# Kernel optimization log

Hardware: AMD Instinct MI355X
Metric: run time of the kernel (lower is better)

The kernel has to match this reference:

```python
import jax, jax.numpy as jnp
import numpy as np

D_MODEL = 512; N_HEADS = 8; HEAD = D_MODEL // N_HEADS; D_FF = 2048
N_LAYERS = 4; VOCAB = 32000; B = 2; S = 1024; T = 1024


def _posenc(seq_len, d_model):
    pos = np.arange(seq_len)[:, None].astype(np.float32)
    div = np.exp(np.arange(0, d_model, 2).astype(np.float32) * (-np.log(10000.0) / d_model))
    pe = np.zeros((seq_len, d_model), dtype=np.float32)
    pe[:, 0::2] = np.sin(pos * div)
    pe[:, 1::2] = np.cos(pos * div)
    return jnp.asarray(pe)


def _layernorm(x, g, b, eps=1e-6):
    mean = x.mean(-1, keepdims=True)
    xc = x - mean
    # torch .var() is unbiased (ddof=1) -- replicate exactly
    var = (xc * xc).sum(-1, keepdims=True) / (x.shape[-1] - 1)
    return g * (xc * (var + eps) ** -0.5) + b


def _mha(q, k, v, w, mask):
    # w: [4, D, D] stacked (W_q, W_k, W_v, W_o), applied as x @ W
    def heads(x, wi):
        return (x @ wi).reshape(x.shape[0], x.shape[1], N_HEADS, HEAD).transpose(0, 2, 1, 3)
    Q, K, V = heads(q, w[0]), heads(k, w[1]), heads(v, w[2])  # [B,H,S,hd]
    att = jnp.einsum('bhqd,bhkd->bhqk', Q, K) * HEAD ** (-0.5)
    att = jnp.where(mask == 0, -jnp.inf, att)
    att = jax.nn.softmax(att, axis=-1)
    y = jnp.einsum('bhqk,bhkd->bhqd', att, V)
    y = y.transpose(0, 2, 1, 3).reshape(q.shape[0], q.shape[1], D_MODEL)
    return y @ w[3]


def _ff(x, w1, b1, w2, b2):
    return jax.nn.relu(x @ w1 + b1) @ w2 + b2


def setup_inputs() -> dict:
    key = jax.random.key(0)
    ks = iter(jax.random.split(key, 32))
    std = 0.02
    inp = {}
    inp['src'] = jax.random.randint(next(ks), (B, S), 0, VOCAB)
    inp['tgt'] = jax.random.randint(next(ks), (B, T), 0, VOCAB)
    inp['src_mask'] = jnp.ones((B, 1, 1, S), dtype=jnp.int32)
    inp['tgt_mask'] = jnp.tril(jnp.ones((T, T), dtype=jnp.int32))[None, None].repeat(B, axis=0)
    inp['src_emb'] = jax.random.normal(next(ks), (VOCAB, D_MODEL)) * std
    inp['tgt_emb'] = jax.random.normal(next(ks), (VOCAB, D_MODEL)) * std
    inp['enc_att_w'] = jax.random.normal(next(ks), (N_LAYERS, 4, D_MODEL, D_MODEL)) * std
    inp['enc_ff_w1'] = jax.random.normal(next(ks), (N_LAYERS, D_MODEL, D_FF)) * std
    inp['enc_ff_b1'] = jnp.zeros((N_LAYERS, D_FF))
    inp['enc_ff_w2'] = jax.random.normal(next(ks), (N_LAYERS, D_FF, D_MODEL)) * std
    inp['enc_ff_b2'] = jnp.zeros((N_LAYERS, D_MODEL))
    inp['enc_norm_g'] = jnp.ones((N_LAYERS, 2, D_MODEL))
    inp['enc_norm_b'] = jnp.zeros((N_LAYERS, 2, D_MODEL))
    inp['enc_final_g'] = jnp.ones((D_MODEL,))
    inp['enc_final_b'] = jnp.zeros((D_MODEL,))
    inp['dec_att_w'] = jax.random.normal(next(ks), (N_LAYERS, 2, 4, D_MODEL, D_MODEL)) * std
    inp['dec_ff_w1'] = jax.random.normal(next(ks), (N_LAYERS, D_MODEL, D_FF)) * std
    inp['dec_ff_b1'] = jnp.zeros((N_LAYERS, D_FF))
    inp['dec_ff_w2'] = jax.random.normal(next(ks), (N_LAYERS, D_FF, D_MODEL)) * std
    inp['dec_ff_b2'] = jnp.zeros((N_LAYERS, D_MODEL))
    inp['dec_norm_g'] = jnp.ones((N_LAYERS, 3, D_MODEL))
    inp['dec_norm_b'] = jnp.zeros((N_LAYERS, 3, D_MODEL))
    inp['dec_final_g'] = jnp.ones((D_MODEL,))
    inp['dec_final_b'] = jnp.zeros((D_MODEL,))
    inp['proj_w'] = jax.random.normal(next(ks), (D_MODEL, VOCAB)) * std
    inp['proj_b'] = jnp.zeros((VOCAB,))
    return inp


def reference(src, tgt, src_mask, tgt_mask, src_emb, tgt_emb,
              enc_att_w, enc_ff_w1, enc_ff_b1, enc_ff_w2, enc_ff_b2,
              enc_norm_g, enc_norm_b, enc_final_g, enc_final_b,
              dec_att_w, dec_ff_w1, dec_ff_b1, dec_ff_w2, dec_ff_b2,
              dec_norm_g, dec_norm_b, dec_final_g, dec_final_b,
              proj_w, proj_b):
    scale = jnp.float32(np.sqrt(D_MODEL))
    # Encoder (pre-norm residuals: x = x + layer(norm(x)); dropout=0)
    x = src_emb[src] * scale + _posenc(S, D_MODEL)[None]
    for i in range(N_LAYERS):
        z = _layernorm(x, enc_norm_g[i, 0], enc_norm_b[i, 0])
        x = x + _mha(z, z, z, enc_att_w[i], src_mask)
        z = _layernorm(x, enc_norm_g[i, 1], enc_norm_b[i, 1])
        x = x + _ff(z, enc_ff_w1[i], enc_ff_b1[i], enc_ff_w2[i], enc_ff_b2[i])
    enc = _layernorm(x, enc_final_g, enc_final_b)
    # Decoder
    y = tgt_emb[tgt] * scale + _posenc(T, D_MODEL)[None]
    for i in range(N_LAYERS):
        z = _layernorm(y, dec_norm_g[i, 0], dec_norm_b[i, 0])
        y = y + _mha(z, z, z, dec_att_w[i, 0], tgt_mask)
        z = _layernorm(y, dec_norm_g[i, 1], dec_norm_b[i, 1])
        y = y + _mha(z, enc, enc, dec_att_w[i, 1], src_mask)
        z = _layernorm(y, dec_norm_g[i, 2], dec_norm_b[i, 2])
        y = y + _ff(z, dec_ff_w1[i], dec_ff_b1[i], dec_ff_w2[i], dec_ff_b2[i])
    dec = _layernorm(y, dec_final_g, dec_final_b)
    return dec @ proj_w + proj_b  # [B, T, VOCAB] logits
```

## Files before the change

### kernel.cpp

```cpp
#include <hip/hip_runtime.h>
#include <hip/hip_bf16.h>
#include <math.h>

#define D_MODEL 512
#define N_HEADS 8
#define HEAD 64
#define D_FF   2048
#define N_LAYERS 4
#define VOCAB  32000
#define BATCH  2
#define SEQ    1024

typedef __attribute__((ext_vector_type(8))) short bf16x8;
typedef __attribute__((ext_vector_type(4))) float f32x4;

__device__ __forceinline__ float b2f(short s) {
    unsigned int u = ((unsigned int)(unsigned short)s) << 16;
    float f; __builtin_memcpy(&f, &u, 4);
    return f;
}
__device__ __forceinline__ short f2b(float f) {
    __hip_bfloat16 h = __float2bfloat16(f);
    unsigned short u; __builtin_memcpy(&u, &h, 2);
    return (short)u;
}
__device__ __forceinline__ void storev(float* p, float v) { *p = v; }
__device__ __forceinline__ void storev(short* p, float v) { *p = f2b(v); }

__device__ __forceinline__ void transT_tile(const float* __restrict__ s,
                                            short* __restrict__ d,
                                            int K, int N, int tx, int ty, int tid) {
    __shared__ float t[64][65];
    int r = tid >> 2, c4 = (tid & 3) * 4;
#pragma unroll
    for (int jj = 0; jj < 4; ++jj) {
        int col = c4 + jj * 16;
        *(float4*)&t[r][col] = *(const float4*)(s + (size_t)(ty * 64 + r) * N + tx * 64 + col);
    }
    __syncthreads();
#pragma unroll
    for (int jj = 0; jj < 4; ++jj) {
        int kc = c4 + jj * 16;
        short4 o = make_short4(f2b(t[kc][r]), f2b(t[kc + 1][r]),
                               f2b(t[kc + 2][r]), f2b(t[kc + 3][r]));
        *(short4*)(d + (size_t)(tx * 64 + r) * K + ty * 64 + kc) = o;
    }
}

__global__ __launch_bounds__(256) void transT_kernel(const float* __restrict__ src,
                                                     short* __restrict__ dst,
                                                     int K, int N) {
    const float* s = src + (size_t)blockIdx.z * K * N;
    short* d = dst + (size_t)blockIdx.z * K * N;
    transT_tile(s, d, K, N, blockIdx.x, blockIdx.y, threadIdx.x);
}

__global__ __launch_bounds__(256) void repack_attT_kernel(const float* __restrict__ encw,
                                                          const float* __restrict__ decw,
                                                          short* __restrict__ w_enc_qkv,
                                                          short* __restrict__ w_dec_qkv,
                                                          short* __restrict__ w_dec_kv,
                                                          short* __restrict__ w_o) {
    int z = blockIdx.y;
    const float* s; short* d;
    if (z < 12)      { int i = z / 3, j = z % 3;
                       s = encw + (size_t)(i * 4 + j) * 262144;
                       d = w_enc_qkv + (size_t)i * 786432 + j * 262144; }
    else if (z < 24) { int u = z - 12, i = u / 3, j = u % 3;
                       s = decw + (size_t)(i * 8 + j) * 262144;
                       d = w_dec_qkv + (size_t)i * 786432 + j * 262144; }
    else if (z < 32) { int u = z - 24, i = u / 2, j = u % 2;
                       s = decw + (size_t)(i * 8 + 5 + j) * 262144;
                       d = w_dec_kv + (size_t)i * 524288 + j * 262144; }
    else             { int u = z - 32; const float* b; int mi;
                       if (u < 4)       { b = encw; mi = u * 4 + 3; }
                       else if (u < 8)  { b = decw; mi = (u - 4) * 8 + 3; }
                       else if (u < 12) { b = decw; mi = (u - 8) * 8 + 4; }
                       else             { b = decw; mi = (u - 12) * 8 + 7; }
                       s = b + (size_t)mi * 262144; d = w_o + (size_t)u * 262144; }
    int bx = blockIdx.x;
    transT_tile(s, d, 512, 512, bx & 7, bx >> 3, threadIdx.x);
}

__global__ void embed_kernel(const int* __restrict__ tokA, const int* __restrict__ tokB,
                             const float* __restrict__ embA, const float* __restrict__ embB,
                             float* __restrict__ outA, float* __restrict__ outB) {
    int row = blockIdx.x;
    const int* tok = blockIdx.y ? tokB : tokA;
    const float* emb = blockIdx.y ? embB : embA;
    float* out = blockIdx.y ? outB : outA;
    int s = row % SEQ;
    int token = tok[row];
    const float scale = 22.627416997969522f;
    const float c = -1.7988945941359737e-2f;
    for (int d = threadIdx.x; d < D_MODEL; d += blockDim.x) {
        int i2 = (d >> 1) * 2;
        float div = expf((float)i2 * c);
        float ang = (float)s * div;
        float pe = (d & 1) ? cosf(ang) : sinf(ang);
        out[(size_t)row * D_MODEL + d] = emb[(size_t)token * D_MODEL + d] * scale + pe;
    }
}

__global__ __launch_bounds__(256) void ln_kernel(const float* __restrict__ x,
                                                 const float* __restrict__ g,
                                                 const float* __restrict__ b,
                                                 short* __restrict__ out) {
    int row = blockIdx.x * 4 + (threadIdx.x >> 6);
    int lane = threadIdx.x & 63;
    const float4* xr = (const float4*)(x + (size_t)row * D_MODEL);
    float4 v0 = xr[lane * 2], v1 = xr[lane * 2 + 1];
    float c[8] = { v0.x, v0.y, v0.z, v0.w, v1.x, v1.y, v1.z, v1.w };
    float s = ((c[0] + c[1]) + (c[2] + c[3])) + ((c[4] + c[5]) + (c[6] + c[7]));
#pragma unroll
    for (int off = 1; off < 64; off <<= 1) s += __shfl_xor(s, off);
    float mean = s * (1.0f / 512.0f);
    float q = 0.0f;
#pragma unroll
    for (int j = 0; j < 8; ++j) { c[j] -= mean; q += c[j] * c[j]; }
#pragma unroll
    for (int off = 1; off < 64; off <<= 1) q += __shfl_xor(q, off);
    float inv = 1.0f / sqrtf(q * (1.0f / 511.0f) + 1e-6f);
    const float4* gp = (const float4*)g;
    const float4* bp = (const float4*)b;
    float4 g0 = gp[lane * 2], g1 = gp[lane * 2 + 1];
    float4 b0 = bp[lane * 2], b1 = bp[lane * 2 + 1];
    float gg[8] = { g0.x, g0.y, g0.z, g0.w, g1.x, g1.y, g1.z, g1.w };
    float bb[8] = { b0.x, b0.y, b0.z, b0.w, b1.x, b1.y, b1.z, b1.w };
    bf16x8 res;
#pragma unroll
    for (int j = 0; j < 8; ++j) res[j] = f2b(gg[j] * (c[j] * inv) + bb[j]);
    *(bf16x8*)(out + (size_t)row * D_MODEL + lane * 8) = res;
}

__global__ __launch_bounds__(256) void mfma_gemm(const short* __restrict__ A,
                                                 const short* __restrict__ WT,
                                                 const float* bias,
                                                 float* __restrict__ C,
                                                 int M, int N, int K) {
    __shared__ __align__(16) short As[128][40];
    __shared__ __align__(16) short Bs[128][40];
    int tid = threadIdx.x;
    int lane = tid & 63, wid = tid >> 6;
    int wm = wid >> 1, wn = wid & 1;
    int gx = gridDim.x;
    int bid = blockIdx.y * gx + blockIdx.x;
    int per = (gx * gridDim.y) >> 3;
    int nb = (bid & 7) * per + (bid >> 3);
    int brow = (nb % gx) * 128;
    int bcol = (nb / gx) * 128;
    int l15 = lane & 15, lk = lane >> 4;

    f32x4 acc[4][4] = {};

    for (int k0 = 0; k0 < K; k0 += 32) {
#pragma unroll
        for (int j = 0; j < 2; ++j) {
            int c = tid + 256 * j;
            int r = c >> 2, seg = (c & 3) * 8;
            *(bf16x8*)&As[r][seg] = *(const bf16x8*)(A  + (size_t)(brow + r) * K + k0 + seg);
            *(bf16x8*)&Bs[r][seg] = *(const bf16x8*)(WT + (size_t)(bcol + r) * K + k0 + seg);
        }
        __syncthreads();
        bf16x8 af[4], bfv[4];
#pragma unroll
        for (int mf = 0; mf < 4; ++mf)
            af[mf] = *(const bf16x8*)&As[64 * wm + 16 * mf + l15][8 * lk];
#pragma unroll
        for (int nf = 0; nf < 4; ++nf)
            bfv[nf] = *(const bf16x8*)&Bs[64 * wn + 16 * nf + l15][8 * lk];
        __builtin_amdgcn_s_setprio(1);
#pragma unroll
        for (int mf = 0; mf < 4; ++mf)
#pragma unroll
            for (int nf = 0; nf < 4; ++nf)
                acc[mf][nf] = __builtin_amdgcn_mfma_f32_16x16x32_bf16(af[mf], bfv[nf], acc[mf][nf], 0, 0, 0);
        __builtin_amdgcn_s_setprio(0);
        __syncthreads();
    }

#pragma unroll
    for (int mf = 0; mf < 4; ++mf) {
#pragma unroll
        for (int nf = 0; nf < 4; ++nf) {
            int n = bcol + 64 * wn + 16 * nf + l15;
            float bv = bias ? bias[n] : 0.0f;
#pragma unroll
            for (int reg = 0; reg < 4; ++reg) {
                int m = brow + 64 * wm + 16 * mf + lk * 4 + reg;
                __builtin_nontemporal_store(acc[mf][nf][reg] + bv, C + (size_t)m * N + n);
            }
        }
    }
}

template <typename OutT>
__global__ __launch_bounds__(256) void mfma_gemm64(const short* __restrict__ A,
                                                   const short* __restrict__ WT,
                                                   const float* bias, const float* resid,
                                                   OutT* __restrict__ C,
                                                   short* __restrict__ vt, int vcol0,
                                                   int M, int N, int K, int relu) {
    __shared__ __align__(16) short As[64][136];
    __shared__ __align__(16) short Bs[64][136];
    int tid = threadIdx.x;
    int lane = tid & 63, wid = tid >> 6;
    int wm = wid >> 1, wn = wid & 1;
    int gx = gridDim.x, gy = gridDim.y;
    int bid = blockIdx.y * gx + blockIdx.x;
    int per = (gx * gy) >> 3;
    int nb = (bid & 7) * per + (bid >> 3);
    int brow = (nb % gy) * 64;
    int bcol = (nb / gy) * 64;
    int l15 = lane & 15, lk = lane >> 4;

    f32x4 acc[2][2] = {};

    int ra = tid >> 2, sa = (tid & 3) * 32;

    for (int k0 = 0; k0 < K; k0 += 128) {
        {
            const short* ab = A + (size_t)(brow + ra) * K + k0 + sa;
            const short* wb = WT + (size_t)(bcol + ra) * K + k0 + sa;
#pragma unroll
            for (int j = 0; j < 4; ++j) {
                *(bf16x8*)&As[ra][sa + 8 * j] = *(const bf16x8*)(ab + 8 * j);
                *(bf16x8*)&Bs[ra][sa + 8 * j] = *(const bf16x8*)(wb + 8 * j);
            }
        }
        __syncthreads();
        __builtin_amdgcn_s_setprio(1);
#pragma unroll
        for (int ks = 0; ks < 4; ++ks) {
            bf16x8 a0 = *(const bf16x8*)&As[32 * wm + l15][32 * ks + 8 * lk];
            bf16x8 a1 = *(const bf16x8*)&As[32 * wm + 16 + l15][32 * ks + 8 * lk];
            bf16x8 b0 = *(const bf16x8*)&Bs[32 * wn + l15][32 * ks + 8 * lk];
            bf16x8 b1 = *(const bf16x8*)&Bs[32 * wn + 16 + l15][32 * ks + 8 * lk];
            acc[0][0] = __builtin_amdgcn_mfma_f32_16x16x32_bf16(a0, b0, acc[0][0], 0, 0, 0);
            acc[0][1] = __builtin_amdgcn_mfma_f32_16x16x32_bf16(a0, b1, acc[0][1], 0, 0, 0);
            acc[1][0] = __builtin_amdgcn_mfma_f32_16x16x32_bf16(a1, b0, acc[1][0], 0, 0, 0);
            acc[1][1] = __builtin_amdgcn_mfma_f32_16x16x32_bf16(a1, b1, acc[1][1], 0, 0, 0);
        }
        __builtin_amdgcn_s_setprio(0);
        __syncthreads();
    }

    if (vt && bcol >= vcol0) {
#pragma unroll
        for (int mf = 0; mf < 2; ++mf) {
#pragma unroll
            for (int nf = 0; nf < 2; ++nf) {
                int rel = bcol + 32 * wn + 16 * nf + l15 - vcol0;
                int hh = rel >> 6, dd = rel & 63;
                int m0 = brow + 32 * wm + 16 * mf + 4 * lk;
                int b = m0 >> 10, k = m0 & 1023;
                short4 o4 = make_short4(f2b(acc[mf][nf][0]), f2b(acc[mf][nf][1]),
                                        f2b(acc[mf][nf][2]), f2b(acc[mf][nf][3]));
                *(short4*)(vt + (((size_t)b * N_HEADS + hh) * HEAD + dd) * SEQ + k) = o4;
            }
        }
        return;
    }

#pragma unroll
    for (int mf = 0; mf < 2; ++mf) {
#pragma unroll
        for (int nf = 0; nf < 2; ++nf) {
            int n = bcol + 32 * wn + 16 * nf + l15;
            float bv = bias ? bias[n] : 0.0f;
#pragma unroll
            for (int reg = 0; reg < 4; ++reg) {
                int m = brow + 32 * wm + 16 * mf + lk * 4 + reg;
                float v = acc[mf][nf][reg] + bv;
                if (resid) v += resid[(size_t)m * N + n];
                if (relu)  v = fmaxf(v, 0.0f);
                storev(C + (size_t)m * N + n, v);
            }
        }
    }
}

__global__ __launch_bounds__(128) void fattn_kernel(const short* __restrict__ Q, int strq,
                                                    const short* __restrict__ Kp, int strkv,
                                                    const short* __restrict__ Vtg,
                                                    short* __restrict__ out, int causal) {
    __shared__ __align__(16) short Ks[64][72];
    __shared__ __align__(16) short Vs[64][72];
    __shared__ __align__(16) short Ps[32][72];
    int tid = threadIdx.x;
    int lane = tid & 63, w = tid >> 6;
    int l15 = lane & 15, lk = lane >> 4;
    int qt = blockIdx.x, h = blockIdx.y, bb = blockIdx.z;
    int q0 = qt * 32;

    bf16x8 qf[2];
    {
        const short* qbase = Q + ((size_t)(bb * SEQ + q0 + 16 * w + l15)) * strq + h * HEAD;
        qf[0] = *(const bf16x8*)(qbase + 8 * lk);
        qf[1] = *(const bf16x8*)(qbase + 32 + 8 * lk);
    }

    f32x4 o[4] = {};
    float lsum = 0.0f;

    int nkt = causal ? ((q0 + 31) / 64 + 1) : (SEQ / 64);
    int rr = tid >> 1, sg = (tid & 1) * 32;
    int qg = q0 + 16 * w + l15;

    const short* vbase = Vtg + (((size_t)bb * N_HEADS + h) * HEAD + rr) * SEQ;

    for (int ktile = 0; ktile < nkt; ++ktile) {
        int k0 = ktile * 64;
        __syncthreads();
        {
            const short* ksrc = Kp + ((size_t)(bb * SEQ + k0 + rr)) * strkv + h * HEAD + sg;
            const short* vsrc = vbase + k0 + sg;
#pragma unroll
            for (int j = 0; j < 4; ++j) {
                *(bf16x8*)&Ks[rr][sg + 8 * j] = *(const bf16x8*)(ksrc + 8 * j);
                *(bf16x8*)&Vs[rr][sg + 8 * j] = *(const bf16x8*)(vsrc + 8 * j);
            }
        }
        __syncthreads();

        f32x4 s[4] = {};
        __builtin_amdgcn_s_setprio(1);
#pragma unroll
        for (int kf = 0; kf < 4; ++kf) {
            bf16x8 k0f = *(const bf16x8*)&Ks[16 * kf + l15][8 * lk];
            bf16x8 k1f = *(const bf16x8*)&Ks[16 * kf + l15][32 + 8 * lk];
            s[kf] = __builtin_amdgcn_mfma_f32_16x16x32_bf16(k0f, qf[0], s[kf], 0, 0, 0);
            s[kf] = __builtin_amdgcn_mfma_f32_16x16x32_bf16(k1f, qf[1], s[kf], 0, 0, 0);
        }
        __builtin_amdgcn_s_setprio(0);

        bool diag = causal && (ktile == nkt - 1);
        float psum = 0.0f;
#pragma unroll
        for (int kf = 0; kf < 4; ++kf) {
            short4 pq;
#pragma unroll
            for (int r = 0; r < 4; ++r) {
                float sv = s[kf][r] * 0.125f;
                if (diag && (k0 + 16 * kf + 4 * lk + r > qg)) sv = -1e30f;
                float p = __expf(sv);
                psum += p;
                ((short*)&pq)[r] = f2b(p);
            }
            *(short4*)&Ps[16 * w + l15][16 * kf + 4 * lk] = pq;
        }
        psum += __shfl_xor(psum, 16);
        psum += __shfl_xor(psum, 32);
        lsum += psum;

        __builtin_amdgcn_s_setprio(1);
#pragma unroll
        for (int ks = 0; ks < 2; ++ks) {
            bf16x8 pb = *(const bf16x8*)&Ps[16 * w + l15][32 * ks + 8 * lk];
#pragma unroll
            for (int df = 0; df < 4; ++df) {
                bf16x8 vf = *(const bf16x8*)&Vs[16 * df + l15][32 * ks + 8 * lk];
                o[df] = __builtin_amdgcn_mfma_f32_16x16x32_bf16(vf, pb, o[df], 0, 0, 0);
            }
        }
        __builtin_amdgcn_s_setprio(0);
    }

    float inv = 1.0f / lsum;
    short* orow = out + ((size_t)(bb * SEQ + qg)) * D_MODEL + h * HEAD;
#pragma unroll
    for (int df = 0; df < 4; ++df) {
        short4 o4 = make_short4(f2b(o[df][0] * inv), f2b(o[df][1] * inv),
                                f2b(o[df][2] * inv), f2b(o[df][3] * inv));
        *(short4*)(orow + 16 * df + 4 * lk) = o4;
    }
}

extern "C" void kernel_launch(void* const* d_in, const int* in_sizes, int n_in,
                              void* d_out, int out_size, void* d_ws, size_t ws_size,
                              hipStream_t stream) {
    const int*   src       = (const int*)  d_in[0];
    const int*   tgt       = (const int*)  d_in[1];
    const float* src_emb   = (const float*)d_in[4];
    const float* tgt_emb   = (const float*)d_in[5];
    const float* enc_att_w = (const float*)d_in[6];
    const float* enc_ff_w1 = (const float*)d_in[7];
    const float* enc_ff_b1 = (const float*)d_in[8];
    const float* enc_ff_w2 = (const float*)d_in[9];
    const float* enc_ff_b2 = (const float*)d_in[10];
    const float* enc_norm_g= (const float*)d_in[11];
    const float* enc_norm_b= (const float*)d_in[12];
    const float* enc_fin_g = (const float*)d_in[13];
    const float* enc_fin_b = (const float*)d_in[14];
    const float* dec_att_w = (const float*)d_in[15];
    const float* dec_ff_w1 = (const float*)d_in[16];
    const float* dec_ff_b1 = (const float*)d_in[17];
    const float* dec_ff_w2 = (const float*)d_in[18];
    const float* dec_ff_b2 = (const float*)d_in[19];
    const float* dec_norm_g= (const float*)d_in[20];
    const float* dec_norm_b= (const float*)d_in[21];
    const float* dec_fin_g = (const float*)d_in[22];
    const float* dec_fin_b = (const float*)d_in[23];
    const float* proj_w    = (const float*)d_in[24];
    const float* proj_b    = (const float*)d_in[25];
    float* out = (float*)d_out;

    const int NROW = BATCH * SEQ;
    const size_t CH = (size_t)NROW * D_MODEL;
    float* ws = (float*)d_ws;
    float* x = ws;
    float* y = x + CH;
    short* z    = (short*)(y + CH);
    short* qkv  = z + CH;
    short* ab   = qkv + 3 * CH;
    short* encb = ab + CH;
    short* ff   = encb + CH;
    short* vt   = ff + 4 * CH;
    short* wts  = vt + CH;

    short* w_enc_qkv = wts;
    short* w_dec_qkv = w_enc_qkv + 4 * 786432;
    short* w_dec_kv  = w_dec_qkv + 4 * 786432;
    short* w_o       = w_dec_kv  + 4 * 524288;
    short* w_enc_ff1 = w_o       + 16 * 262144;
    short* w_enc_ff2 = w_enc_ff1 + 4194304;
    short* w_dec_ff1 = w_enc_ff2 + 4194304;
    short* w_dec_ff2 = w_dec_ff1 + 4194304;
    short* w_proj    = w_dec_ff2 + 4194304;

    {
        dim3 ga(64, 48);
        repack_attT_kernel<<<ga, 256, 0, stream>>>(enc_att_w, dec_att_w,
                                                   w_enc_qkv, w_dec_qkv, w_dec_kv, w_o);
        dim3 gf1(D_FF / 64, D_MODEL / 64, 4);
        transT_kernel<<<gf1, 256, 0, stream>>>(enc_ff_w1, w_enc_ff1, D_MODEL, D_FF);
        transT_kernel<<<gf1, 256, 0, stream>>>(dec_ff_w1, w_dec_ff1, D_MODEL, D_FF);
        dim3 gf2(D_MODEL / 64, D_FF / 64, 4);
        transT_kernel<<<gf2, 256, 0, stream>>>(enc_ff_w2, w_enc_ff2, D_FF, D_MODEL);
        transT_kernel<<<gf2, 256, 0, stream>>>(dec_ff_w2, w_dec_ff2, D_FF, D_MODEL);
        dim3 gp(VOCAB / 64, D_MODEL / 64);
        transT_kernel<<<gp, 256, 0, stream>>>(proj_w, w_proj, D_MODEL, VOCAB);
    }

    auto g64_b = [&](const short* A, const short* W, const float* bias, const float* resid,
                     short* C, short* vto, int vcol0, int M, int N, int K, int relu) {
        dim3 g(N / 64, M / 64);
        mfma_gemm64<short><<<g, 256, 0, stream>>>(A, W, bias, resid, C, vto, vcol0, M, N, K, relu);
    };
    auto g64_f = [&](const short* A, const short* W, const float* bias, const float* resid,
                     float* C, int M, int N, int K, int relu) {
        dim3 g(N / 64, M / 64);
        mfma_gemm64<float><<<g, 256, 0, stream>>>(A, W, bias, resid, C, nullptr, 0, M, N, K, relu);
    };
    auto ln = [&](const float* in, const float* g, const float* b, short* outp) {
        ln_kernel<<<NROW / 4, 256, 0, stream>>>(in, g, b, outp);
    };
    auto attn = [&](const short* Q, int strq, const short* K, int strkv, short* O, int causal) {
        dim3 g(SEQ / 32, N_HEADS, BATCH);
        fattn_kernel<<<g, 128, 0, stream>>>(Q, strq, K, strkv, vt, O, causal);
    };

    {
        dim3 ge(NROW, 2);
        embed_kernel<<<ge, 256, 0, stream>>>(src, tgt, src_emb, tgt_emb, x, y);
    }
    for (int i = 0; i < N_LAYERS; ++i) {
        ln(x, enc_norm_g + (i * 2 + 0) * D_MODEL, enc_norm_b + (i * 2 + 0) * D_MODEL, z);
        g64_b(z, w_enc_qkv + (size_t)i * 786432, nullptr, nullptr, qkv, vt, 1024, NROW, 1536, D_MODEL, 0);
        attn(qkv, 1536, qkv + 512, 1536, ab, 0);
        g64_f(ab, w_o + (size_t)i * 262144, nullptr, x, x, NROW, D_MODEL, D_MODEL, 0);
        ln(x, enc_norm_g + (i * 2 + 1) * D_MODEL, enc_norm_b + (i * 2 + 1) * D_MODEL, z);
        g64_b(z, w_enc_ff1 + (size_t)i * 1048576, enc_ff_b1 + i * D_FF, nullptr, ff, nullptr, 0, NROW, D_FF, D_MODEL, 1);
        g64_f(ff, w_enc_ff2 + (size_t)i * 1048576, enc_ff_b2 + i * D_MODEL, x, x, NROW, D_MODEL, D_FF, 0);
    }
    ln(x, enc_fin_g, enc_fin_b, encb);

    for (int i = 0; i < N_LAYERS; ++i) {
        ln(y, dec_norm_g + (i * 3 + 0) * D_MODEL, dec_norm_b + (i * 3 + 0) * D_MODEL, z);
        g64_b(z, w_dec_qkv + (size_t)i * 786432, nullptr, nullptr, qkv, vt, 1024, NROW, 1536, D_MODEL, 0);
        attn(qkv, 1536, qkv + 512, 1536, ab, 1);
        g64_f(ab, w_o + (size_t)(4 + i) * 262144, nullptr, y, y, NROW, D_MODEL, D_MODEL, 0);
        ln(y, dec_norm_g + (i * 3 + 1) * D_MODEL, dec_norm_b + (i * 3 + 1) * D_MODEL, z);
        {
            short* crossq = qkv;
            short* kv     = qkv + CH;
            g64_b(z,    w_o + (size_t)(8 + i) * 262144, nullptr, nullptr, crossq, nullptr, 0, NROW, D_MODEL, D_MODEL, 0);
            g64_b(encb, w_dec_kv + (size_t)i * 524288,  nullptr, nullptr, kv, vt, 512, NROW, 1024, D_MODEL, 0);
            attn(crossq, 512, kv, 1024, ab, 0);
        }
        g64_f(ab, w_o + (size_t)(12 + i) * 262144, nullptr, y, y, NROW, D_MODEL, D_MODEL, 0);
        ln(y, dec_norm_g + (i * 3 + 2) * D_MODEL, dec_norm_b + (i * 3 + 2) * D_MODEL, z);
        g64_b(z, w_dec_ff1 + (size_t)i * 1048576, dec_ff_b1 + i * D_FF, nullptr, ff, nullptr, 0, NROW, D_FF, D_MODEL, 1);
        g64_f(ff, w_dec_ff2 + (size_t)i * 1048576, dec_ff_b2 + i * D_MODEL, y, y, NROW, D_MODEL, D_FF, 0);
    }
    ln(y, dec_fin_g, dec_fin_b, z);

    dim3 pg(NROW / 128, VOCAB / 128);
    mfma_gemm<<<pg, 256, 0, stream>>>(z, w_proj, proj_b, out, NROW, VOCAB, D_MODEL);
}
```

Before: 1.149 ms.

## Fuse LayerNorm into GEMM A-operand loads and add 128x128 tiled GEMM

Removes the separate LayerNorm kernels by computing per-row mean and inverse std inside the GEMM prologue. The fp32 activations are then normalized and converted to bf16 while the A tiles are staged into shared memory. A new 128x128-tile GEMM handles the QKV, FF1 and cross-attention KV projections, with a mixed epilogue that writes transposed V. The encoder final norm is recomputed in every decoder layer's KV projection rather than materialised once. This trades extra redundant LN arithmetic and fp32 reads (each N-tile re-normalises the same rows) for fewer launches and less intermediate traffic.

```diff
diff --git a/kernel.cpp b/kernel.cpp
--- a/kernel.cpp
+++ b/kernel.cpp
@@ -195,11 +195,162 @@
 }
 
 template <typename OutT>
-__global__ __launch_bounds__(256) void mfma_gemm64(const short* __restrict__ A,
+__global__ __launch_bounds__(256) void gemm128_ln(const float* __restrict__ A,
+                                                  const float* __restrict__ lng,
+                                                  const float* __restrict__ lnb,
+                                                  const short* __restrict__ WT,
+                                                  const float* bias, const float* resid,
+                                                  OutT* __restrict__ C,
+                                                  short* __restrict__ vt, int vcol0,
+                                                  int M, int N, int relu) {
+    __shared__ __align__(16) short As[128][72];
+    __shared__ __align__(16) short Bs[128][72];
+    __shared__ float sg[512], sb[512], smean[128], sinv[128];
+    const int K = 512;
+    int tid = threadIdx.x;
+    int lane = tid & 63, wid = tid >> 6;
+    int wm = wid >> 1, wn = wid & 1;
+    int gx = gridDim.x;
+    int bid = blockIdx.y * gx + blockIdx.x;
+    int per = (gx * gridDim.y) >> 3;
+    int nb = (bid & 7) * per + (bid >> 3);
+    int brow = (nb % gx) * 128;
+    int bcol = (nb / gx) * 128;
+    int l15 = lane & 15, lk = lane >> 4;
+
+    if (tid < 128) {
+        ((float4*)sg)[tid] = ((const float4*)lng)[tid];
+        ((float4*)sb)[tid] = ((const float4*)lnb)[tid];
+    }
+#pragma unroll
+    for (int p = 0; p < 8; ++p) {
+        int r = (tid >> 4) + 16 * p;
+        const float* xr = A + (size_t)(brow + r) * K + 8 * (tid & 15);
+        float s = 0.0f, q = 0.0f;
+#pragma unroll
+        for (int cc = 0; cc < 4; ++cc) {
+            float4 a  = *(const float4*)(xr + 128 * cc);
+            float4 b4 = *(const float4*)(xr + 128 * cc + 4);
+            s += ((a.x + a.y) + (a.z + a.w)) + ((b4.x + b4.y) + (b4.z + b4.w));
+            q += a.x*a.x + a.y*a.y + a.z*a.z + a.w*a.w
+               + b4.x*b4.x + b4.y*b4.y + b4.z*b4.z + b4.w*b4.w;
+        }
+#pragma unroll
+        for (int off = 1; off < 16; off <<= 1) {
+            s += __shfl_xor(s, off);
+            q += __shfl_xor(q, off);
+        }
+        if ((tid & 15) == 0) {
+            float mean = s * (1.0f / 512.0f);
+            smean[r] = mean;
+            sinv[r] = 1.0f / sqrtf((q - 512.0f * mean * mean) * (1.0f / 511.0f) + 1e-6f);
+        }
+    }
+    __syncthreads();
+
+    f32x4 acc[4][4] = {};
+
+    for (int k0 = 0; k0 < K; k0 += 64) {
+#pragma unroll
+        for (int j = 0; j < 2; ++j) {
+            int c = tid + 256 * j;
+            int r = c >> 2, seg = (c & 3) * 16;
+            const float* xp = A + (size_t)(brow + r) * K + k0 + seg;
+            float mean = smean[r], inv = sinv[r];
+            bf16x8 o0, o1;
+#pragma unroll
+            for (int e = 0; e < 8; ++e) {
+                int kk = k0 + seg + e;
+                o0[e] = f2b(sg[kk] * ((xp[e] - mean) * inv) + sb[kk]);
+            }
+#pragma unroll
+            for (int e = 0; e < 8; ++e) {
+                int kk = k0 + seg + 8 + e;
+                o1[e] = f2b(sg[kk] * ((xp[8 + e] - mean) * inv) + sb[kk]);
+            }
+            *(bf16x8*)&As[r][seg] = o0;
+            *(bf16x8*)&As[r][seg + 8] = o1;
+        }
+#pragma unroll
+        for (int j = 0; j < 4; ++j) {
+            int c = tid + 256 * j;
+            int r = c >> 3, seg = (c & 7) * 8;
+            *(bf16x8*)&Bs[r][seg] = *(const bf16x8*)(WT + (size_t)(bcol + r) * K + k0 + seg);
+        }
+        __syncthreads();
+#pragma unroll
+        for (int ks = 0; ks < 2; ++ks) {
+            bf16x8 af[4], bfv[4];
+#pragma unroll
+            for (int mf = 0; mf < 4; ++mf)
+                af[mf] = *(const bf16x8*)&As[64 * wm + 16 * mf + l15][32 * ks + 8 * lk];
+#pragma unroll
+            for (int nf = 0; nf < 4; ++nf)
+                bfv[nf] = *(const bf16x8*)&Bs[64 * wn + 16 * nf + l15][32 * ks + 8 * lk];
+            __builtin_amdgcn_s_setprio(1);
+#pragma unroll
+            for (int mf = 0; mf < 4; ++mf)
+#pragma unroll
+                for (int nf = 0; nf < 4; ++nf)
+                    acc[mf][nf] = __builtin_amdgcn_mfma_f32_16x16x32_bf16(af[mf], bfv[nf], acc[mf][nf], 0, 0, 0);
+            __builtin_amdgcn_s_setprio(0);
+        }
+        __syncthreads();
+    }
+
+    if (vt && bcol + 128 > vcol0) {
+#pragma unroll
+        for (int mf = 0; mf < 4; ++mf) {
+#pragma unroll
+            for (int nf = 0; nf < 4; ++nf) {
+                int n = bcol + 64 * wn + 16 * nf + l15;
+                if (n < vcol0) {
+                    float bv = bias ? bias[n] : 0.0f;
+#pragma unroll
+                    for (int reg = 0; reg < 4; ++reg) {
+                        int m = brow + 64 * wm + 16 * mf + lk * 4 + reg;
+                        float v = acc[mf][nf][reg] + bv;
+                        storev(C + (size_t)m * N + n, v);
+                    }
+                } else {
+                    int rel = n - vcol0;
+                    int hh = rel >> 6, dd = rel & 63;
+                    int m0 = brow + 64 * wm + 16 * mf + 4 * lk;
+                    int b = m0 >> 10, k = m0 & 1023;
+                    short4 o4 = make_short4(f2b(acc[mf][nf][0]), f2b(acc[mf][nf][1]),
+                                            f2b(acc[mf][nf][2]), f2b(acc[mf][nf][3]));
+                    *(short4*)(vt + (((size_t)b * N_HEADS + hh) * HEAD + dd) * SEQ + k) = o4;
+                }
+            }
+        }
+        return;
+    }
+
+#pragma unroll
+    for (int mf = 0; mf < 4; ++mf) {
+#pragma unroll
+        for (int nf = 0; nf < 4; ++nf) {
+            int n = bcol + 64 * wn + 16 * nf + l15;
+            float bv = bias ? bias[n] : 0.0f;
+#pragma unroll
+            for (int reg = 0; reg < 4; ++reg) {
+                int m = brow + 64 * wm + 16 * mf + lk * 4 + reg;
+                float v = acc[mf][nf][reg] + bv;
+                if (resid) v += resid[(size_t)m * N + n];
+                if (relu)  v = fmaxf(v, 0.0f);
+                storev(C + (size_t)m * N + n, v);
+            }
+        }
+    }
+}
+
+template <typename OutT, int LNA>
+__global__ __launch_bounds__(256) void mfma_gemm64(const void* __restrict__ Av,
+                                                   const float* __restrict__ lng,
+                                                   const float* __restrict__ lnb,
                                                    const short* __restrict__ WT,
                                                    const float* bias, const float* resid,
                                                    OutT* __restrict__ C,
-                                                   short* __restrict__ vt, int vcol0,
                                                    int M, int N, int K, int relu) {
     __shared__ __align__(16) short As[64][136];
     __shared__ __align__(16) short Bs[64][136];
@@ -214,19 +365,69 @@
     int bcol = (nb / gy) * 64;
     int l15 = lane & 15, lk = lane >> 4;
 
+    __shared__ float sg[512], sb[512], smean[64], sinv[64];
+    if constexpr (LNA) {
+        if (tid < 128) {
+            ((float4*)sg)[tid] = ((const float4*)lng)[tid];
+            ((float4*)sb)[tid] = ((const float4*)lnb)[tid];
+        }
+        const float* Af = (const float*)Av;
+#pragma unroll
+        for (int p = 0; p < 4; ++p) {
+            int r = (tid >> 4) + 16 * p;
+            const float* xr = Af + (size_t)(brow + r) * 512 + 8 * (tid & 15);
+            float s = 0.0f, q = 0.0f;
+#pragma unroll
+            for (int cc = 0; cc < 4; ++cc) {
+                float4 a  = *(const float4*)(xr + 128 * cc);
+                float4 b4 = *(const float4*)(xr + 128 * cc + 4);
+                s += ((a.x + a.y) + (a.z + a.w)) + ((b4.x + b4.y) + (b4.z + b4.w));
+                q += a.x*a.x + a.y*a.y + a.z*a.z + a.w*a.w
+                   + b4.x*b4.x + b4.y*b4.y + b4.z*b4.z + b4.w*b4.w;
+            }
+#pragma unroll
+            for (int off = 1; off < 16; off <<= 1) {
+                s += __shfl_xor(s, off);
+                q += __shfl_xor(q, off);
+            }
+            if ((tid & 15) == 0) {
+                float mean = s * (1.0f / 512.0f);
+                smean[r] = mean;
+                sinv[r] = 1.0f / sqrtf((q - 512.0f * mean * mean) * (1.0f / 511.0f) + 1e-6f);
+            }
+        }
+        __syncthreads();
+    }
+
     f32x4 acc[2][2] = {};
 
     int ra = tid >> 2, sa = (tid & 3) * 32;
 
     for (int k0 = 0; k0 < K; k0 += 128) {
+        if constexpr (LNA) {
+            const float* xp = (const float*)Av + (size_t)(brow + ra) * 512 + k0 + sa;
+            float mean = smean[ra], inv = sinv[ra];
+#pragma unroll
+            for (int j = 0; j < 4; ++j) {
+                bf16x8 o;
+#pragma unroll
+                for (int e = 0; e < 8; ++e) {
+                    int kk = k0 + sa + 8 * j + e;
+                    o[e] = f2b(sg[kk] * ((xp[8 * j + e] - mean) * inv) + sb[kk]);
+                }
+                *(bf16x8*)&As[ra][sa + 8 * j] = o;
+            }
+        } else {
+            const short* ab = (const short*)Av + (size_t)(brow + ra) * K + k0 + sa;
+#pragma unroll
+            for (int j = 0; j < 4; ++j)
+                *(bf16x8*)&As[ra][sa + 8 * j] = *(const bf16x8*)(ab + 8 * j);
+        }
         {
-            const short* ab = A + (size_t)(brow + ra) * K + k0 + sa;
             const short* wb = WT + (size_t)(bcol + ra) * K + k0 + sa;
 #pragma unroll
-            for (int j = 0; j < 4; ++j) {
-                *(bf16x8*)&As[ra][sa + 8 * j] = *(const bf16x8*)(ab + 8 * j);
+            for (int j = 0; j < 4; ++j)
                 *(bf16x8*)&Bs[ra][sa + 8 * j] = *(const bf16x8*)(wb + 8 * j);
-            }
         }
         __syncthreads();
         __builtin_amdgcn_s_setprio(1);
@@ -243,23 +444,6 @@
         }
         __builtin_amdgcn_s_setprio(0);
         __syncthreads();
-    }
-
-    if (vt && bcol >= vcol0) {
-#pragma unroll
-        for (int mf = 0; mf < 2; ++mf) {
-#pragma unroll
-            for (int nf = 0; nf < 2; ++nf) {
-                int rel = bcol + 32 * wn + 16 * nf + l15 - vcol0;
-                int hh = rel >> 6, dd = rel & 63;
-                int m0 = brow + 32 * wm + 16 * mf + 4 * lk;
-                int b = m0 >> 10, k = m0 & 1023;
-                short4 o4 = make_short4(f2b(acc[mf][nf][0]), f2b(acc[mf][nf][1]),
-                                        f2b(acc[mf][nf][2]), f2b(acc[mf][nf][3]));
-                *(short4*)(vt + (((size_t)b * N_HEADS + hh) * HEAD + dd) * SEQ + k) = o4;
-            }
-        }
-        return;
     }
 
 #pragma unroll
@@ -442,18 +626,21 @@
         transT_kernel<<<gp, 256, 0, stream>>>(proj_w, w_proj, D_MODEL, VOCAB);
     }
 
-    auto g64_b = [&](const short* A, const short* W, const float* bias, const float* resid,
-                     short* C, short* vto, int vcol0, int M, int N, int K, int relu) {
+    auto g128 = [&](const float* A, const float* lg, const float* lb, const short* W,
+                    const float* bias, const float* resid, short* C,
+                    short* vto, int vcol0, int M, int N, int relu) {
+        dim3 g(M / 128, N / 128);
+        gemm128_ln<short><<<g, 256, 0, stream>>>(A, lg, lb, W, bias, resid, C, vto, vcol0, M, N, relu);
+    };
+    auto g64_plain_f = [&](const short* A, const short* W, const float* bias, const float* resid,
+                           float* C, int M, int N, int K, int relu) {
         dim3 g(N / 64, M / 64);
-        mfma_gemm64<short><<<g, 256, 0, stream>>>(A, W, bias, resid, C, vto, vcol0, M, N, K, relu);
+        mfma_gemm64<float, 0><<<g, 256, 0, stream>>>(A, nullptr, nullptr, W, bias, resid, C, M, N, K, relu);
     };
-    auto g64_f = [&](const short* A, const short* W, const float* bias, const float* resid,
-                     float* C, int M, int N, int K, int relu) {
+    auto g64_ln_b = [&](const float* A, const float* lg, const float* lb, const short* W,
+                        short* C, int M, int N) {
         dim3 g(N / 64, M / 64);
-        mfma_gemm64<float><<<g, 256, 0, stream>>>(A, W, bias, resid, C, nullptr, 0, M, N, K, relu);
-    };
-    auto ln = [&](const float* in, const float* g, const float* b, short* outp) {
-        ln_kernel<<<NROW / 4, 256, 0, stream>>>(in, g, b, outp);
+        mfma_gemm64<short, 1><<<g, 256, 0, stream>>>(A, lg, lb, W, nullptr, nullptr, C, M, N, 512, 0);
     };
     auto attn = [&](const short* Q, int strq, const short* K, int strkv, short* O, int causal) {
         dim3 g(SEQ / 32, N_HEADS, BATCH);
@@ -464,36 +651,37 @@
         dim3 ge(NROW, 2);
         embed_kernel<<<ge, 256, 0, stream>>>(src, tgt, src_emb, tgt_emb, x, y);
     }
+
     for (int i = 0; i < N_LAYERS; ++i) {
-        ln(x, enc_norm_g + (i * 2 + 0) * D_MODEL, enc_norm_b + (i * 2 + 0) * D_MODEL, z);
-        g64_b(z, w_enc_qkv + (size_t)i * 786432, nullptr, nullptr, qkv, vt, 1024, NROW, 1536, D_MODEL, 0);
+        g128(x, enc_norm_g + (i * 2 + 0) * D_MODEL, enc_norm_b + (i * 2 + 0) * D_MODEL,
+             w_enc_qkv + (size_t)i * 786432, nullptr, nullptr, qkv, vt, 1024, NROW, 1536, 0);
         attn(qkv, 1536, qkv + 512, 1536, ab, 0);
-        g64_f(ab, w_o + (size_t)i * 262144, nullptr, x, x, NROW, D_MODEL, D_MODEL, 0);
-        ln(x, enc_norm_g + (i * 2 + 1) * D_MODEL, enc_norm_b + (i * 2 + 1) * D_MODEL, z);
-        g64_b(z, w_enc_ff1 + (size_t)i * 1048576, enc_ff_b1 + i * D_FF, nullptr, ff, nullptr, 0, NROW, D_FF, D_MODEL, 1);
-        g64_f(ff, w_enc_ff2 + (size_t)i * 1048576, enc_ff_b2 + i * D_MODEL, x, x, NROW, D_MODEL, D_FF, 0);
-    }
-    ln(x, enc_fin_g, enc_fin_b, encb);
+        g64_plain_f(ab, w_o + (size_t)i * 262144, nullptr, x, x, NROW, D_MODEL, D_MODEL, 0);
+        g128(x, enc_norm_g + (i * 2 + 1) * D_MODEL, enc_norm_b + (i * 2 + 1) * D_MODEL,
+             w_enc_ff1 + (size_t)i * 1048576, enc_ff_b1 + i * D_FF, nullptr, ff, nullptr, 1 << 30, NROW, D_FF, 1);
+        g64_plain_f(ff, w_enc_ff2 + (size_t)i * 1048576, enc_ff_b2 + i * D_MODEL, x, x, NROW, D_MODEL, D_FF, 0);
+    }
 
     for (int i = 0; i < N_LAYERS; ++i) {
-        ln(y, dec_norm_g + (i * 3 + 0) * D_MODEL, dec_norm_b + (i * 3 + 0) * D_MODEL, z);
-        g64_b(z, w_dec_qkv + (size_t)i * 786432, nullptr, nullptr, qkv, vt, 1024, NROW, 1536, D_MODEL, 0);
+        g128(y, dec_norm_g + (i * 3 + 0) * D_MODEL, dec_norm_b + (i * 3 + 0) * D_MODEL,
+             w_dec_qkv + (size_t)i * 786432, nullptr, nullptr, qkv, vt, 1024, NROW, 1536, 0);
         attn(qkv, 1536, qkv + 512, 1536, ab, 1);
-        g64_f(ab, w_o + (size_t)(4 + i) * 262144, nullptr, y, y, NROW, D_MODEL, D_MODEL, 0);
-        ln(y, dec_norm_g + (i * 3 + 1) * D_MODEL, dec_norm_b + (i * 3 + 1) * D_MODEL, z);
+        g64_plain_f(ab, w_o + (size_t)(4 + i) * 262144, nullptr, y, y, NROW, D_MODEL, D_MODEL, 0);
         {
             short* crossq = qkv;
             short* kv     = qkv + CH;
-            g64_b(z,    w_o + (size_t)(8 + i) * 262144, nullptr, nullptr, crossq, nullptr, 0, NROW, D_MODEL, D_MODEL, 0);
-            g64_b(encb, w_dec_kv + (size_t)i * 524288,  nullptr, nullptr, kv, vt, 512, NROW, 1024, D_MODEL, 0);
+            g64_ln_b(y, dec_norm_g + (i * 3 + 1) * D_MODEL, dec_norm_b + (i * 3 + 1) * D_MODEL,
+                     w_o + (size_t)(8 + i) * 262144, crossq, NROW, D_MODEL);
+            g128(x, enc_fin_g, enc_fin_b, w_dec_kv + (size_t)i * 524288,
+                 nullptr, nullptr, kv, vt, 512, NROW, 1024, 0);
             attn(crossq, 512, kv, 1024, ab, 0);
         }
-        g64_f(ab, w_o + (size_t)(12 + i) * 262144, nullptr, y, y, NROW, D_MODEL, D_MODEL, 0);
-        ln(y, dec_norm_g + (i * 3 + 2) * D_MODEL, dec_norm_b + (i * 3 + 2) * D_MODEL, z);
-        g64_b(z, w_dec_ff1 + (size_t)i * 1048576, dec_ff_b1 + i * D_FF, nullptr, ff, nullptr, 0, NROW, D_FF, D_MODEL, 1);
-        g64_f(ff, w_dec_ff2 + (size_t)i * 1048576, dec_ff_b2 + i * D_MODEL, y, y, NROW, D_MODEL, D_FF, 0);
-    }
-    ln(y, dec_fin_g, dec_fin_b, z);
+        g64_plain_f(ab, w_o + (size_t)(12 + i) * 262144, nullptr, y, y, NROW, D_MODEL, D_MODEL, 0);
+        g128(y, dec_norm_g + (i * 3 + 2) * D_MODEL, dec_norm_b + (i * 3 + 2) * D_MODEL,
+             w_dec_ff1 + (size_t)i * 1048576, dec_ff_b1 + i * D_FF, nullptr, ff, nullptr, 1 << 30, NROW, D_FF, 1);
+        g64_plain_f(ff, w_dec_ff2 + (size_t)i * 1048576, dec_ff_b2 + i * D_MODEL, y, y, NROW, D_MODEL, D_FF, 0);
+    }
+    ln_kernel<<<NROW / 4, 256, 0, stream>>>(y, dec_fin_g, dec_fin_b, z);
 
     dim3 pg(NROW / 128, VOCAB / 128);
     mfma_gemm<<<pg, 256, 0, stream>>>(z, w_proj, proj_b, out, NROW, VOCAB, D_MODEL);
```

Result: slower. 1.376 ms (+19.8%).

## Split-K residual GEMMs with atomic float accumulation into residual stream

Applied to the files above, without the earlier changes.

The output-projection and FF2 GEMMs, which have N=512 and so launch few blocks, now split K across gridDim.z (2 or 4 slices). Each slice atomically adds its partial tile, plus the bias from the first slice only, directly into the fp32 residual buffer. This replaces the separate residual read-and-write and raises block count to fill more CUs. The cost is atomic traffic and a summation order that is no longer deterministic. The decoder LN call is only moved inside a scope block, with no change in ordering.

```diff
diff --git a/kernel.cpp b/kernel.cpp
--- a/kernel.cpp
+++ b/kernel.cpp
@@ -194,7 +194,7 @@
     }
 }
 
-template <typename OutT>
+template <typename OutT, int ATOMIC>
 __global__ __launch_bounds__(256) void mfma_gemm64(const short* __restrict__ A,
                                                    const short* __restrict__ WT,
                                                    const float* bias, const float* resid,
@@ -214,11 +214,15 @@
     int bcol = (nb / gy) * 64;
     int l15 = lane & 15, lk = lane >> 4;
 
+    int kz = ATOMIC ? blockIdx.z : 0;
+    int kper = ATOMIC ? (K / gridDim.z) : K;
+    int kbeg = kz * kper, kend = kbeg + kper;
+
     f32x4 acc[2][2] = {};
 
     int ra = tid >> 2, sa = (tid & 3) * 32;
 
-    for (int k0 = 0; k0 < K; k0 += 128) {
+    for (int k0 = kbeg; k0 < kend; k0 += 128) {
         {
             const short* ab = A + (size_t)(brow + ra) * K + k0 + sa;
             const short* wb = WT + (size_t)(bcol + ra) * K + k0 + sa;
@@ -243,6 +247,24 @@
         }
         __builtin_amdgcn_s_setprio(0);
         __syncthreads();
+    }
+
+    if constexpr (ATOMIC) {
+        float* Cf = (float*)C;
+#pragma unroll
+        for (int mf = 0; mf < 2; ++mf) {
+#pragma unroll
+            for (int nf = 0; nf < 2; ++nf) {
+                int n = bcol + 32 * wn + 16 * nf + l15;
+                float bv = (kz == 0 && bias) ? bias[n] : 0.0f;
+#pragma unroll
+                for (int reg = 0; reg < 4; ++reg) {
+                    int m = brow + 32 * wm + 16 * mf + lk * 4 + reg;
+                    atomicAdd(Cf + (size_t)m * N + n, acc[mf][nf][reg] + bv);
+                }
+            }
+        }
+        return;
     }
 
     if (vt && bcol >= vcol0) {
@@ -445,12 +467,12 @@
     auto g64_b = [&](const short* A, const short* W, const float* bias, const float* resid,
                      short* C, short* vto, int vcol0, int M, int N, int K, int relu) {
         dim3 g(N / 64, M / 64);
-        mfma_gemm64<short><<<g, 256, 0, stream>>>(A, W, bias, resid, C, vto, vcol0, M, N, K, relu);
+        mfma_gemm64<short, 0><<<g, 256, 0, stream>>>(A, W, bias, resid, C, vto, vcol0, M, N, K, relu);
     };
-    auto g64_f = [&](const short* A, const short* W, const float* bias, const float* resid,
-                     float* C, int M, int N, int K, int relu) {
-        dim3 g(N / 64, M / 64);
-        mfma_gemm64<float><<<g, 256, 0, stream>>>(A, W, bias, resid, C, nullptr, 0, M, N, K, relu);
+    auto g64_atomic = [&](const short* A, const short* W, const float* bias,
+                          float* C, int M, int N, int K, int split) {
+        dim3 g(N / 64, M / 64, split);
+        mfma_gemm64<float, 1><<<g, 256, 0, stream>>>(A, W, bias, nullptr, C, nullptr, 0, M, N, K, 0);
     };
     auto ln = [&](const float* in, const float* g, const float* b, short* outp) {
         ln_kernel<<<NROW / 4, 256, 0, stream>>>(in, g, b, outp);
@@ -464,14 +486,15 @@
         dim3 ge(NROW, 2);
         embed_kernel<<<ge, 256, 0, stream>>>(src, tgt, src_emb, tgt_emb, x, y);
     }
+
     for (int i = 0; i < N_LAYERS; ++i) {
         ln(x, enc_norm_g + (i * 2 + 0) * D_MODEL, enc_norm_b + (i * 2 + 0) * D_MODEL, z);
         g64_b(z, w_enc_qkv + (size_t)i * 786432, nullptr, nullptr, qkv, vt, 1024, NROW, 1536, D_MODEL, 0);
         attn(qkv, 1536, qkv + 512, 1536, ab, 0);
-        g64_f(ab, w_o + (size_t)i * 262144, nullptr, x, x, NROW, D_MODEL, D_MODEL, 0);
+        g64_atomic(ab, w_o + (size_t)i * 262144, nullptr, x, NROW, D_MODEL, D_MODEL, 2);
         ln(x, enc_norm_g + (i * 2 + 1) * D_MODEL, enc_norm_b + (i * 2 + 1) * D_MODEL, z);
         g64_b(z, w_enc_ff1 + (size_t)i * 1048576, enc_ff_b1 + i * D_FF, nullptr, ff, nullptr, 0, NROW, D_FF, D_MODEL, 1);
-        g64_f(ff, w_enc_ff2 + (size_t)i * 1048576, enc_ff_b2 + i * D_MODEL, x, x, NROW, D_MODEL, D_FF, 0);
+        g64_atomic(ff, w_enc_ff2 + (size_t)i * 1048576, enc_ff_b2 + i * D_MODEL, x, NROW, D_MODEL, D_FF, 4);
     }
     ln(x, enc_fin_g, enc_fin_b, encb);
 
@@ -479,19 +502,19 @@
         ln(y, dec_norm_g + (i * 3 + 0) * D_MODEL, dec_norm_b + (i * 3 + 0) * D_MODEL, z);
         g64_b(z, w_dec_qkv + (size_t)i * 786432, nullptr, nullptr, qkv, vt, 1024, NROW, 1536, D_MODEL, 0);
         attn(qkv, 1536, qkv + 512, 1536, ab, 1);
-        g64_f(ab, w_o + (size_t)(4 + i) * 262144, nullptr, y, y, NROW, D_MODEL, D_MODEL, 0);
-        ln(y, dec_norm_g + (i * 3 + 1) * D_MODEL, dec_norm_b + (i * 3 + 1) * D_MODEL, z);
+        g64_atomic(ab, w_o + (size_t)(4 + i) * 262144, nullptr, y, NROW, D_MODEL, D_MODEL, 2);
         {
             short* crossq = qkv;
             short* kv     = qkv + CH;
-            g64_b(z,    w_o + (size_t)(8 + i) * 262144, nullptr, nullptr, crossq, nullptr, 0, NROW, D_MODEL, D_MODEL, 0);
-            g64_b(encb, w_dec_kv + (size_t)i * 524288,  nullptr, nullptr, kv, vt, 512, NROW, 1024, D_MODEL, 0);
+            ln(y, dec_norm_g + (i * 3 + 1) * D_MODEL, dec_norm_b + (i * 3 + 1) * D_MODEL, z);
+            g64_b(z, w_o + (size_t)(8 + i) * 262144, nullptr, nullptr, crossq, nullptr, 0, NROW, D_MODEL, D_MODEL, 0);
+            g64_b(encb, w_dec_kv + (size_t)i * 524288, nullptr, nullptr, kv, vt, 512, NROW, 1024, D_MODEL, 0);
             attn(crossq, 512, kv, 1024, ab, 0);
         }
-        g64_f(ab, w_o + (size_t)(12 + i) * 262144, nullptr, y, y, NROW, D_MODEL, D_MODEL, 0);
+        g64_atomic(ab, w_o + (size_t)(12 + i) * 262144, nullptr, y, NROW, D_MODEL, D_MODEL, 2);
         ln(y, dec_norm_g + (i * 3 + 2) * D_MODEL, dec_norm_b + (i * 3 + 2) * D_MODEL, z);
         g64_b(z, w_dec_ff1 + (size_t)i * 1048576, dec_ff_b1 + i * D_FF, nullptr, ff, nullptr, 0, NROW, D_FF, D_MODEL, 1);
-        g64_f(ff, w_dec_ff2 + (size_t)i * 1048576, dec_ff_b2 + i * D_MODEL, y, y, NROW, D_MODEL, D_FF, 0);
+        g64_atomic(ff, w_dec_ff2 + (size_t)i * 1048576, dec_ff_b2 + i * D_MODEL, y, NROW, D_MODEL, D_FF, 4);
     }
     ln(y, dec_fin_g, dec_fin_b, z);
 
```

New measurement: 1.111 ms. 1.03x faster.
